# Kernel optimization log

Measured on AMD Instinct MI355X. Metric: run time of the kernel, lower is better.

## Reference

```python
import jax, jax.numpy as jnp
import numpy as np

INPUT_SIZE, HIDDEN_SIZE, MEMORY_SIZE, SEQ_LEN, THETA = 512, 1024, 256, 4096, 4096.0
BATCH = 8


def _expm(M):
    # scaling-and-squaring Taylor expm (float64), replaces scipy cont2discrete's expm
    nrm = np.linalg.norm(M, 1)
    s = max(0, int(np.ceil(np.log2(max(nrm, 1.0)))) + 4)
    A = M / (2.0 ** s)
    E = np.eye(M.shape[0])
    T = np.eye(M.shape[0])
    for k in range(1, 24):
        T = T @ A / k
        E = E + T
    for _ in range(s):
        E = E @ E
    return E


def _lmu_H():
    # continuous-time Legendre state-space matrices
    Q = np.arange(MEMORY_SIZE, dtype=np.float64).reshape(-1, 1)
    R = (2.0 * Q + 1.0) / THETA
    i, j = np.meshgrid(Q.ravel(), Q.ravel(), indexing="ij")
    A = R * np.where(i < j, -1.0, (-1.0) ** (i - j + 1))
    B = R * (-1.0) ** Q
    # zero-order-hold discretization with dt=1: expm([[A,B],[0,0]])
    aug = np.zeros((MEMORY_SIZE + 1, MEMORY_SIZE + 1))
    aug[:MEMORY_SIZE, :MEMORY_SIZE] = A
    aug[:MEMORY_SIZE, MEMORY_SIZE:] = B
    Md = _expm(aug)
    Ad = Md[:MEMORY_SIZE, :MEMORY_SIZE].astype(np.float32)
    Bd = Md[:MEMORY_SIZE, MEMORY_SIZE:].astype(np.float32)
    # impulse response: H[:, t] = Ad^t @ Bd  (matches torch impulse() in float32)
    H = np.empty((MEMORY_SIZE, SEQ_LEN), dtype=np.float32)
    h = Bd[:, 0]
    for t in range(SEQ_LEN):
        H[:, t] = h
        h = Ad @ h
    return H


def setup_inputs():
    key = jax.random.key(0)
    k1, k2, k3, k4, k5 = jax.random.split(key, 5)
    x = jax.random.normal(k1, (BATCH, SEQ_LEN, INPUT_SIZE), jnp.float32)
    W_u_w = jax.random.normal(k2, (1, INPUT_SIZE), jnp.float32) / np.float32(np.sqrt(INPUT_SIZE))
    W_u_b = jax.random.normal(k3, (1,), jnp.float32) * 0.01
    W_h_w = jax.random.normal(k4, (HIDDEN_SIZE, MEMORY_SIZE + INPUT_SIZE), jnp.float32) / np.float32(np.sqrt(MEMORY_SIZE + INPUT_SIZE))
    W_h_b = jax.random.normal(k5, (HIDDEN_SIZE,), jnp.float32) * 0.01
    H = jnp.asarray(_lmu_H())
    return {"x": x, "W_u_w": W_u_w, "W_u_b": W_u_b, "W_h_w": W_h_w, "W_h_b": W_h_b, "H": H}


def reference(x, W_u_w, W_u_b, W_h_w, W_h_b, H):
    B, S, D = x.shape
    # u_t = relu(W_u x_t)  -> [B, S, 1]
    u = jax.nn.relu(jnp.einsum("bsd,od->bso", x, W_u_w) + W_u_b)
    # FFT long convolution of u with impulse response H (linear conv via 2S padding)
    fft_u = jnp.fft.rfft(u.transpose(0, 2, 1), n=2 * S, axis=-1)  # [B, 1, S+1]
    fft_H = jnp.fft.rfft(H, n=2 * S, axis=-1)                     # [M, S+1]
    m = jnp.fft.irfft(fft_u * fft_H[None], n=2 * S, axis=-1)[:, :, :S]  # [B, M, S]
    m = m.transpose(0, 2, 1)                                      # [B, S, M]
    # h_t = relu(W_h [m_t; x_t])
    h = jax.nn.relu(jnp.einsum("bsk,hk->bsh", jnp.concatenate([m, x], axis=-1), W_h_w) + W_h_b)
    return h, h[:, -1, :]
```

## Files before the change

kernel.cpp:

```cpp
#include <hip/hip_runtime.h>

typedef _Float16 half8 __attribute__((ext_vector_type(8)));
typedef float f32x4 __attribute__((ext_vector_type(4)));

#define SEQ   4096
#define DIN   512
#define HID   1024
#define KMEM  256
#define NB    8
#define KC    768
#define VP    4352
#define OUT_H_ELEMS 33554432ull

__device__ __forceinline__ void load_lds16(const void* g, void* l) {
  __builtin_amdgcn_global_load_lds(
      (const __attribute__((address_space(1))) unsigned int*)g,
      (__attribute__((address_space(3))) unsigned int*)l, 16, 0, 0);
}

__global__ __launch_bounds__(256) void u_kernel(
    const float* __restrict__ x, const float* __restrict__ Wu,
    const float* __restrict__ Wub,
    const float* __restrict__ Hf, const float* __restrict__ Wf,
    _Float16* __restrict__ xh, _Float16* __restrict__ v2,
    _Float16* __restrict__ Hh, _Float16* __restrict__ Wh)
{
  int tid_g = blockIdx.x * 256 + threadIdx.x;
  if (tid_g < KMEM * SEQ) Hh[tid_g] = (_Float16)Hf[tid_g];
  if (tid_g < HID * KC)   Wh[tid_g] = (_Float16)Wf[tid_g];
  if (tid_g < NB * 8 * 256) {
    int b2 = tid_g >> 11, rem = tid_g & 2047, p = rem >> 8, z = rem & 255;
    int t = (z < p) ? z : 4096 + z;
    v2[((size_t)b2 * 8 + p) * VP + t] = (_Float16)0.f;
  }

  int w = threadIdx.x >> 6, lane = threadIdx.x & 63;
  int row = blockIdx.x * 4 + w;
  const float4* xr = (const float4*)(x + (size_t)row * DIN);
  const float4* wr = (const float4*)Wu;
  float4 a0 = xr[lane * 2], a1 = xr[lane * 2 + 1];
  float4 w0 = wr[lane * 2], w1 = wr[lane * 2 + 1];
  float dot = a0.x * w0.x + a0.y * w0.y + a0.z * w0.z + a0.w * w0.w
            + a1.x * w1.x + a1.y * w1.y + a1.z * w1.z + a1.w * w1.w;
  half8 hv;
  hv[0] = (_Float16)a0.x; hv[1] = (_Float16)a0.y;
  hv[2] = (_Float16)a0.z; hv[3] = (_Float16)a0.w;
  hv[4] = (_Float16)a1.x; hv[5] = (_Float16)a1.y;
  hv[6] = (_Float16)a1.z; hv[7] = (_Float16)a1.w;
  *((half8*)(xh + (size_t)row * DIN + lane * 8)) = hv;
  #pragma unroll
  for (int off = 32; off > 0; off >>= 1) dot += __shfl_xor(dot, off);
  float u = dot + Wub[0];
  u = u > 0.f ? u : 0.f;
  if (lane < 8) {
    int s = row & (SEQ - 1), b = row >> 12;
    v2[(size_t)b * 8 * VP + (size_t)lane * VP + (4095 - s + lane)] = (_Float16)u;
  }
}

__global__ __launch_bounds__(256, 3) void conv_kernel(
    const _Float16* __restrict__ Hh, const _Float16* __restrict__ v2,
    _Float16* __restrict__ mh)
{
  __shared__ _Float16 Bs[2][128 * 64];
  __shared__ _Float16 Aw[2][8 * 208];
  int g = blockIdx.x;
  int cb = g & 15;
  int b = cb >> 1, kt = cb & 1;
  int jj = g >> 4;
  int its = (jj < 16) ? jj : (47 - jj);
  int s0 = its * 128, k0 = kt * 128;
  int tid = threadIdx.x;
  int w = tid >> 6, lane = tid & 63;
  int wr = w >> 1, wc = w & 1;
  int lm = lane & 15, q = lane >> 4;
  const _Float16* v2b = v2 + (size_t)b * 8 * VP;
  int gb = 3968 - s0;

  int aoffs[4];
  #pragma unroll
  for (int mi = 0; mi < 4; mi++) {
    int X = wr * 64 + mi * 16 + lm;
    int p = (X + 1) & 7;
    aoffs[mi] = p * 208 + (127 - X + p) + q * 8;
  }
  int boffs[4];
  #pragma unroll
  for (int ni = 0; ni < 4; ni++) {
    int col = wc * 64 + ni * 16 + lm;
    boffs[ni] = col * 64 + ((q ^ (lm & 7)) << 3);
  }

  int ap = tid / 26, aidx = tid - ap * 26;

  f32x4 acc[4][4] = {};
  int iters = 2 * (its + 1);

  {
    if (tid < 208)
      load_lds16(v2b + (size_t)ap * VP + gb + aidx * 8, Aw[0] + tid * 8);
    #pragma unroll
    for (int p2 = 0; p2 < 4; p2++) {
      int c = p2 * 256 + tid;
      int col = c >> 3, sl = c & 7;
      load_lds16(Hh + (size_t)(k0 + col) * SEQ + ((sl ^ (col & 7)) << 3),
                 Bs[0] + (size_t)c * 8);
    }
  }

  for (int it = 0; it < iters; ++it) {
    int buf = it & 1;
    __syncthreads();
    if (it + 1 < iters) {
      int r0 = (it + 1) * 64;
      if (tid < 208)
        load_lds16(v2b + (size_t)ap * VP + gb + r0 + aidx * 8, Aw[buf ^ 1] + tid * 8);
      #pragma unroll
      for (int p2 = 0; p2 < 4; p2++) {
        int c = p2 * 256 + tid;
        int col = c >> 3, sl = c & 7;
        load_lds16(Hh + (size_t)(k0 + col) * SEQ + r0 + ((sl ^ (col & 7)) << 3),
                   Bs[buf ^ 1] + (size_t)c * 8);
      }
    }
    #pragma unroll
    for (int kq = 0; kq < 2; kq++) {
      half8 af[4], bf[4];
      #pragma unroll
      for (int mi = 0; mi < 4; mi++)
        af[mi] = *((const half8*)(Aw[buf] + aoffs[mi] + kq * 32));
      #pragma unroll
      for (int ni = 0; ni < 4; ni++)
        bf[ni] = *((const half8*)(Bs[buf] + (boffs[ni] ^ (kq << 5))));
      #pragma unroll
      for (int mi = 0; mi < 4; mi++)
        #pragma unroll
        for (int ni = 0; ni < 4; ni++)
          acc[mi][ni] = __builtin_amdgcn_mfma_f32_16x16x32_f16(af[mi], bf[ni], acc[mi][ni], 0, 0, 0);
    }
  }
  size_t rowbase = (size_t)b * SEQ;
  #pragma unroll
  for (int mi = 0; mi < 4; mi++) {
    #pragma unroll
    for (int ni = 0; ni < 4; ni++) {
      int kout = k0 + wc * 64 + ni * 16 + lm;
      #pragma unroll
      for (int r = 0; r < 4; r++) {
        int sout = s0 + wr * 64 + mi * 16 + q * 4 + r;
        mh[(rowbase + sout) * KMEM + kout] = (_Float16)acc[mi][ni][r];
      }
    }
  }
}

__global__ __launch_bounds__(512, 2) void h_kernel(
    const _Float16* __restrict__ mh, const _Float16* __restrict__ xh,
    const _Float16* __restrict__ Wh, const float* __restrict__ Whb,
    float* __restrict__ out)
{
  __shared__ _Float16 A3[3][256 * 32];
  __shared__ _Float16 B3[3][256 * 32];

  int id = blockIdx.x;
  int wgid = (id & 7) * 64 + (id >> 3);
  int mt = wgid >> 2, nt = wgid & 3;

  int tid = threadIdx.x;
  int w = tid >> 6, lane = tid & 63;
  int wr = w >> 2, wc = w & 3;
  int lm = lane & 15, q = lane >> 4;

  int offM[2], offX[2], offB[2], ldsc[2];
  #pragma unroll
  for (int r = 0; r < 2; ++r) {
    int row = r * 128 + (tid >> 2);
    int sl = tid & 3;
    offM[r] = (mt * 256 + row) * KMEM + sl * 8;
    offX[r] = (mt * 256 + row) * DIN  + sl * 8;
    offB[r] = (nt * 256 + row) * KC   + sl * 8;
    ldsc[r] = (r * 512 + tid) * 8;
  }

#define H_STAGE(t) do {                                                        \
    const int kk_ = (t) * 32;                                                  \
    _Float16* As_ = A3[(t) % 3];                                               \
    _Float16* Bs_ = B3[(t) % 3];                                               \
    _Pragma("unroll")                                                          \
    for (int r_ = 0; r_ < 2; ++r_) {                                           \
      const _Float16* sa_ = (kk_ < KMEM) ? (mh + offM[r_] + kk_)               \
                                         : (xh + offX[r_] + (kk_ - KMEM));     \
      load_lds16(sa_, As_ + ldsc[r_]);                                         \
      load_lds16(Wh + offB[r_] + kk_, Bs_ + ldsc[r_]);                         \
    }                                                                          \
  } while (0)

  f32x4 acc[8][4] = {};

  H_STAGE(0); H_STAGE(1);
  asm volatile("s_waitcnt vmcnt(4)" ::: "memory");
  __builtin_amdgcn_s_barrier();
  asm volatile("" ::: "memory");

  #pragma unroll
  for (int t = 0; t < 24; ++t) {
    if (t + 2 < 24) H_STAGE(t + 2);
    const _Float16* la = A3[t % 3];
    const _Float16* lb = B3[t % 3];
    half8 af[8], bf[4];
    #pragma unroll
    for (int mi = 0; mi < 8; ++mi)
      af[mi] = *((const half8*)(la + (wr * 128 + mi * 16 + lm) * 32 + q * 8));
    #pragma unroll
    for (int ni = 0; ni < 4; ++ni)
      bf[ni] = *((const half8*)(lb + (wc * 64 + ni * 16 + lm) * 32 + q * 8));
    __builtin_amdgcn_s_setprio(1);
    #pragma unroll
    for (int mi = 0; mi < 8; ++mi)
      #pragma unroll
      for (int ni = 0; ni < 4; ++ni)
        acc[mi][ni] = __builtin_amdgcn_mfma_f32_16x16x32_f16(af[mi], bf[ni], acc[mi][ni], 0, 0, 0);
    __builtin_amdgcn_s_setprio(0);
    asm volatile("" ::: "memory");
    if (t < 22)       asm volatile("s_waitcnt vmcnt(4)" ::: "memory");
    else if (t == 22) asm volatile("s_waitcnt vmcnt(0)" ::: "memory");
    if (t < 23) {
      __builtin_amdgcn_s_barrier();
      asm volatile("" ::: "memory");
    }
  }
#undef H_STAGE

  #pragma unroll
  for (int ni = 0; ni < 4; ++ni) {
    int colg = nt * 256 + wc * 64 + ni * 16 + lm;
    float bias = Whb[colg];
    #pragma unroll
    for (int mi = 0; mi < 8; ++mi) {
      #pragma unroll
      for (int r = 0; r < 4; ++r) {
        int rowg = mt * 256 + wr * 128 + mi * 16 + q * 4 + r;
        float v = acc[mi][ni][r] + bias;
        v = v > 0.f ? v : 0.f;
        out[(size_t)rowg * HID + colg] = v;
        if ((rowg & (SEQ - 1)) == SEQ - 1)
          out[OUT_H_ELEMS + (size_t)(rowg >> 12) * HID + colg] = v;
      }
    }
  }
}

extern "C" void kernel_launch(void* const* d_in, const int* in_sizes, int n_in,
                              void* d_out, int out_size, void* d_ws, size_t ws_size,
                              hipStream_t stream) {
  const float* x   = (const float*)d_in[0];
  const float* Wu  = (const float*)d_in[1];
  const float* Wub = (const float*)d_in[2];
  const float* Whw = (const float*)d_in[3];
  const float* Whb = (const float*)d_in[4];
  const float* Hf  = (const float*)d_in[5];
  float* out = (float*)d_out;

  char* ws = (char*)d_ws;
  _Float16* Hh = (_Float16*)(ws);
  _Float16* Wh = (_Float16*)(ws + 2097152);
  _Float16* v2 = (_Float16*)(ws + 3670016);
  _Float16* xh = (_Float16*)(ws + 4227072);
  _Float16* mh = (_Float16*)(ws + 37781504);

  u_kernel<<<dim3(8192), dim3(256), 0, stream>>>(x, Wu, Wub, Hf, Whw, xh, v2, Hh, Wh);
  conv_kernel<<<dim3(512), dim3(256), 0, stream>>>(Hh, v2, mh);
  h_kernel<<<dim3(512), dim3(512), 0, stream>>>(mh, xh, Wh, Whb, out);
}
```

Before: 338.0 us.

## Retile h_kernel to 128x128 blocks with swizzled LDS and nontemporal stores

The output GEMM moves from 256x256 tiles with 512 threads to 128x128 tiles with 256 threads, launching 2048 blocks with an XCD-aware block-to-tile mapping. An XOR swizzle is applied to the LDS chunk layout to avoid bank conflicts on fragment reads, and the output is written with nontemporal stores. Smaller tiles improve occupancy and load balance, but they lower arithmetic intensity and add global traffic for operand reloads.

```diff
diff --git a/kernel.cpp b/kernel.cpp
--- a/kernel.cpp
+++ b/kernel.cpp
@@ -154,33 +154,39 @@
   }
 }
 
-__global__ __launch_bounds__(512, 2) void h_kernel(
+__global__ __launch_bounds__(256, 3) void h_kernel(
     const _Float16* __restrict__ mh, const _Float16* __restrict__ xh,
     const _Float16* __restrict__ Wh, const float* __restrict__ Whb,
     float* __restrict__ out)
 {
-  __shared__ _Float16 A3[3][256 * 32];
-  __shared__ _Float16 B3[3][256 * 32];
-
-  int id = blockIdx.x;
-  int wgid = (id & 7) * 64 + (id >> 3);
-  int mt = wgid >> 2, nt = wgid & 3;
-
-  int tid = threadIdx.x;
-  int w = tid >> 6, lane = tid & 63;
-  int wr = w >> 2, wc = w & 3;
-  int lm = lane & 15, q = lane >> 4;
-
-  int offM[2], offX[2], offB[2], ldsc[2];
+  __shared__ _Float16 A3[3][128 * 32];
+  __shared__ _Float16 B3[3][128 * 32];
+  int id = blockIdx.y * 8 + blockIdx.x;
+  int xcd = id & 7;
+  int j = id >> 3;
+  int mt = (j >> 3) * 8 + xcd;
+  int nt = j & 7;
+  int tid = threadIdx.x, w = tid >> 6, lane = tid & 63;
+  int wr = w >> 1, wc = w & 1, lm = lane & 15, q = lane >> 4;
+
+  int offM[2], offX[2], offB[2], ldsoff[2];
   #pragma unroll
   for (int r = 0; r < 2; ++r) {
-    int row = r * 128 + (tid >> 2);
-    int sl = tid & 3;
-    offM[r] = (mt * 256 + row) * KMEM + sl * 8;
-    offX[r] = (mt * 256 + row) * DIN  + sl * 8;
-    offB[r] = (nt * 256 + row) * KC   + sl * 8;
-    ldsc[r] = (r * 512 + tid) * 8;
-  }
+    int c = r * 256 + tid;
+    int row = c >> 2, ch = c & 3;
+    int sw = ch ^ ((row >> 2) & 3);
+    offM[r] = (mt * 128 + row) * KMEM + sw * 8;
+    offX[r] = (mt * 128 + row) * DIN  + sw * 8;
+    offB[r] = (nt * 128 + row) * KC   + sw * 8;
+    ldsoff[r] = c * 8;
+  }
+
+  int qs = (q ^ ((lm >> 2) & 3)) << 3;
+  int aoff[4], boff[4];
+  #pragma unroll
+  for (int mi = 0; mi < 4; ++mi) aoff[mi] = (wr * 64 + mi * 16 + lm) * 32 + qs;
+  #pragma unroll
+  for (int ni = 0; ni < 4; ++ni) boff[ni] = (wc * 64 + ni * 16 + lm) * 32 + qs;
 
 #define H_STAGE(t) do {                                                        \
     const int kk_ = (t) * 32;                                                  \
@@ -190,12 +196,12 @@
     for (int r_ = 0; r_ < 2; ++r_) {                                           \
       const _Float16* sa_ = (kk_ < KMEM) ? (mh + offM[r_] + kk_)               \
                                          : (xh + offX[r_] + (kk_ - KMEM));     \
-      load_lds16(sa_, As_ + ldsc[r_]);                                         \
-      load_lds16(Wh + offB[r_] + kk_, Bs_ + ldsc[r_]);                         \
+      load_lds16(sa_, As_ + ldsoff[r_]);                                       \
+      load_lds16(Wh + offB[r_] + kk_, Bs_ + ldsoff[r_]);                       \
     }                                                                          \
   } while (0)
 
-  f32x4 acc[8][4] = {};
+  f32x4 acc[4][4] = {};
 
   H_STAGE(0); H_STAGE(1);
   asm volatile("s_waitcnt vmcnt(4)" ::: "memory");
@@ -207,16 +213,14 @@
     if (t + 2 < 24) H_STAGE(t + 2);
     const _Float16* la = A3[t % 3];
     const _Float16* lb = B3[t % 3];
-    half8 af[8], bf[4];
-    #pragma unroll
-    for (int mi = 0; mi < 8; ++mi)
-      af[mi] = *((const half8*)(la + (wr * 128 + mi * 16 + lm) * 32 + q * 8));
-    #pragma unroll
-    for (int ni = 0; ni < 4; ++ni)
-      bf[ni] = *((const half8*)(lb + (wc * 64 + ni * 16 + lm) * 32 + q * 8));
+    half8 af[4], bf[4];
+    #pragma unroll
+    for (int mi = 0; mi < 4; ++mi) af[mi] = *((const half8*)(la + aoff[mi]));
+    #pragma unroll
+    for (int ni = 0; ni < 4; ++ni) bf[ni] = *((const half8*)(lb + boff[ni]));
     __builtin_amdgcn_s_setprio(1);
     #pragma unroll
-    for (int mi = 0; mi < 8; ++mi)
+    for (int mi = 0; mi < 4; ++mi)
       #pragma unroll
       for (int ni = 0; ni < 4; ++ni)
         acc[mi][ni] = __builtin_amdgcn_mfma_f32_16x16x32_f16(af[mi], bf[ni], acc[mi][ni], 0, 0, 0);
@@ -232,19 +236,20 @@
 #undef H_STAGE
 
   #pragma unroll
-  for (int ni = 0; ni < 4; ++ni) {
-    int colg = nt * 256 + wc * 64 + ni * 16 + lm;
+  for (int ni = 0; ni < 4; ni++) {
+    int colg = nt * 128 + wc * 64 + ni * 16 + lm;
     float bias = Whb[colg];
     #pragma unroll
-    for (int mi = 0; mi < 8; ++mi) {
-      #pragma unroll
-      for (int r = 0; r < 4; ++r) {
-        int rowg = mt * 256 + wr * 128 + mi * 16 + q * 4 + r;
+    for (int mi = 0; mi < 4; mi++) {
+      #pragma unroll
+      for (int r = 0; r < 4; r++) {
+        int rowg = mt * 128 + wr * 64 + mi * 16 + q * 4 + r;
         float v = acc[mi][ni][r] + bias;
         v = v > 0.f ? v : 0.f;
-        out[(size_t)rowg * HID + colg] = v;
+        __builtin_nontemporal_store(v, &out[(size_t)rowg * HID + colg]);
         if ((rowg & (SEQ - 1)) == SEQ - 1)
-          out[OUT_H_ELEMS + (size_t)(rowg >> 12) * HID + colg] = v;
+          __builtin_nontemporal_store(
+              v, &out[OUT_H_ELEMS + (size_t)(rowg >> 12) * HID + colg]);
       }
     }
   }
@@ -270,5 +275,5 @@
 
   u_kernel<<<dim3(8192), dim3(256), 0, stream>>>(x, Wu, Wub, Hf, Whw, xh, v2, Hh, Wh);
   conv_kernel<<<dim3(512), dim3(256), 0, stream>>>(Hh, v2, mh);
-  h_kernel<<<dim3(512), dim3(512), 0, stream>>>(mh, xh, Wh, Whb, out);
-}
+  h_kernel<<<dim3(8, 256), dim3(256), 0, stream>>>(mh, xh, Wh, Whb, out);
+}
```

New measurement: 308.8 us. 8.6% less time.
